# Kernel optimization log

Hardware: AMD Instinct MI355X
Metric: run time of the kernel (lower is better)

Reference implementation:

```python
import jax, jax.numpy as jnp
import numpy as np

NUM_ROUTES = 32
LN_EPS = 1e-5


def _ln(x, g, b):
    mu = jnp.mean(x, axis=-1, keepdims=True)
    var = jnp.mean(jnp.square(x - mu), axis=-1, keepdims=True)
    return (x - mu) * jax.lax.rsqrt(var + LN_EPS) * g + b


def setup_inputs() -> dict:
    key = jax.random.key(0)
    ks = jax.random.split(key, 16)
    B, N, D = 64, 512, 512
    s = 1.0 / np.sqrt(D)
    return {
        "tokens": jax.random.normal(ks[0], (B, N, D), jnp.float32),
        "token_mask": jax.random.bernoulli(ks[1], 0.7, (B, N)),
        "route_ids": jax.random.randint(ks[2], (N,), 0, NUM_ROUTES),
        # token_ffn: LayerNorm + Linear(D,4D) + GELU + Linear(4D,D)
        "ln1_g": jnp.ones((D,), jnp.float32),
        "ln1_b": jnp.zeros((D,), jnp.float32),
        "w1": jax.random.normal(ks[3], (D, 4 * D), jnp.float32) * s,
        "b1": jnp.zeros((4 * D,), jnp.float32),
        "w2": jax.random.normal(ks[4], (4 * D, D), jnp.float32) * (0.5 * s),
        "b2": jnp.zeros((D,), jnp.float32),
        # within_route_pool: LayerNorm + Linear(D,1)
        "wp_g": jnp.ones((D,), jnp.float32),
        "wp_b": jnp.zeros((D,), jnp.float32),
        "wp_w": jax.random.normal(ks[5], (D,), jnp.float32) * s,
        "wp_bias": jnp.zeros((), jnp.float32),
        # route_pool: LayerNorm + Linear(D,1)
        "rp_g": jnp.ones((D,), jnp.float32),
        "rp_b": jnp.zeros((D,), jnp.float32),
        "rp_w": jax.random.normal(ks[6], (D,), jnp.float32) * s,
        "rp_bias": jnp.zeros((), jnp.float32),
    }


def reference(tokens, token_mask, route_ids, ln1_g, ln1_b, w1, b1, w2, b2,
              wp_g, wp_b, wp_w, wp_bias, rp_g, rp_b, rp_w, rp_bias):
    # token FFN with residual (dropout=0 in eval path)
    h = _ln(tokens, ln1_g, ln1_b)
    h = jax.nn.gelu(h @ w1 + b1, approximate=False)
    x = tokens + (h @ w2 + b2)                       # [B, N, D]

    # within-route attention pool: score is mask-independent -> compute once
    tok_logits = _ln(x, wp_g, wp_b) @ wp_w + wp_bias  # [B, N]

    route_onehot = route_ids[None, :] == jnp.arange(NUM_ROUTES)[:, None]  # [R, N]
    mask = route_onehot[None, :, :] & token_mask[:, None, :]              # [B, R, N]

    ml = jnp.where(mask, tok_logits[:, None, :], -1e9)
    w = jax.nn.softmax(ml, axis=-1)
    w = jnp.where(mask, w, 0.0)
    w = w / jnp.maximum(jnp.sum(w, axis=-1, keepdims=True), 1e-6)
    routes = jnp.einsum('brn,bnd->brd', w, x)         # [B, R, D]
    present = jnp.any(mask, axis=-1)                  # [B, R]

    # route-level attention pool
    rl = _ln(routes, rp_g, rp_b) @ rp_w + rp_bias     # [B, R]
    rl = jnp.where(present, rl, -1e9)
    rw = jax.nn.softmax(rl, axis=-1)
    rw = jnp.where(present, rw, 0.0)
    rw = rw / jnp.maximum(jnp.sum(rw, axis=-1, keepdims=True), 1e-6)
    return jnp.einsum('br,brd->bd', rw, routes)       # [B, D]
```

## Files before the change

kernel.cpp:

```cpp
#include <hip/hip_runtime.h>
#include <hip/hip_bf16.h>
#include <math.h>

#define B_ 64
#define N_ 512
#define D_ 512
#define H_ 2048
#define R_ 32
#define M_ (B_ * N_)

typedef __bf16 bf16x8 __attribute__((ext_vector_type(8)));
typedef float f32x4 __attribute__((ext_vector_type(4)));

__device__ __forceinline__ void async_ld16(const void* g, void* l) {
  __builtin_amdgcn_global_load_lds((__attribute__((address_space(1))) void*)g,
                                   (__attribute__((address_space(3))) void*)l,
                                   16, 0, 0);
}

__device__ __forceinline__ float fast_gelu(float v) {
  const float s = v * 0.70710678118654752f;
  const float a = fabsf(s);
  const float t = 1.0f / fmaf(0.3275911f, a, 1.0f);
  const float poly = t * fmaf(t, fmaf(t, fmaf(t, fmaf(t, 1.061405429f, -1.453152027f),
                                              1.421413741f), -0.284496736f), 0.254829592f);
  const float er = 1.0f - poly * __expf(-a * a);
  const float erfs = (s >= 0.f) ? er : -er;
  return 0.5f * v * (1.0f + erfs);
}

__global__ void mask_detect_kernel(const unsigned char* __restrict__ raw,
                                   int* __restrict__ flag) {
  __shared__ int f;
  if (threadIdx.x == 0) f = 0;
  __syncthreads();
  const uint4* p = (const uint4*)raw;
  unsigned acc = 0;
  for (int k = threadIdx.x; k < M_ / 16; k += 256) {
    const uint4 v = p[k];
    acc |= (v.x | v.y | v.z | v.w) & 0xFFFFFF00u;
  }
  if (acc) f = 1;
  __syncthreads();
  if (threadIdx.x == 0) flag[0] = f;
}

__global__ __launch_bounds__(256) void transpose_cast_kernel(
    const float* __restrict__ src, __hip_bfloat16* __restrict__ dst, int R, int C) {
  __shared__ float tile[64][65];
  const int c0 = blockIdx.x * 64, r0 = blockIdx.y * 64;
  const int tx = threadIdx.x & 63, ty = threadIdx.x >> 6;
  for (int r = ty; r < 64; r += 4)
    tile[r][tx] = src[(size_t)(r0 + r) * C + c0 + tx];
  __syncthreads();
  for (int r = ty; r < 64; r += 4)
    dst[(size_t)(c0 + r) * R + r0 + tx] = __float2bfloat16(tile[tx][r]);
}

__global__ __launch_bounds__(512) void ln_rows_kernel(
    const float* __restrict__ src, const float* __restrict__ gw,
    const float* __restrict__ gb, __hip_bfloat16* __restrict__ dst) {
  const int wv = threadIdx.x >> 6, lane = threadIdx.x & 63;
  const int row = blockIdx.x * 8 + wv;
  const float* p = src + (size_t)row * D_ + lane * 8;
  const float4 v0 = *(const float4*)p;
  const float4 v1 = *(const float4*)(p + 4);
  float s = v0.x + v0.y + v0.z + v0.w + v1.x + v1.y + v1.z + v1.w;
  float ss = v0.x * v0.x + v0.y * v0.y + v0.z * v0.z + v0.w * v0.w +
             v1.x * v1.x + v1.y * v1.y + v1.z * v1.z + v1.w * v1.w;
#pragma unroll
  for (int m = 32; m > 0; m >>= 1) {
    s += __shfl_xor(s, m);
    ss += __shfl_xor(ss, m);
  }
  const float mu = s * (1.0f / D_);
  const float rstd = rsqrtf(ss * (1.0f / D_) - mu * mu + 1e-5f);
  const float4 g0 = *(const float4*)(gw + lane * 8);
  const float4 g1 = *(const float4*)(gw + lane * 8 + 4);
  const float4 b0 = *(const float4*)(gb + lane * 8);
  const float4 b1 = *(const float4*)(gb + lane * 8 + 4);
  const float vv[8] = {v0.x, v0.y, v0.z, v0.w, v1.x, v1.y, v1.z, v1.w};
  const float gg[8] = {g0.x, g0.y, g0.z, g0.w, g1.x, g1.y, g1.z, g1.w};
  const float bb[8] = {b0.x, b0.y, b0.z, b0.w, b1.x, b1.y, b1.z, b1.w};
  union { __hip_bfloat16 h[8]; uint4 u; } pk;
#pragma unroll
  for (int t = 0; t < 8; ++t)
    pk.h[t] = __float2bfloat16((vv[t] - mu) * rstd * gg[t] + bb[t]);
  *(uint4*)(dst + (size_t)row * D_ + lane * 8) = pk.u;
}

__global__ __launch_bounds__(256, 2) void gemm_bias_gelu_kernel(
    const __hip_bfloat16* __restrict__ A, const __hip_bfloat16* __restrict__ Bt,
    const float* __restrict__ bias, __hip_bfloat16* __restrict__ C,
    int K, int ldc, int NC) {
  __shared__ alignas(16) unsigned short SU[8192];
  unsigned short* As = SU;
  unsigned short* Bs = SU + 4096;
  const int tid = threadIdx.x;
  const int w = tid >> 6;
  const int lane = tid & 63;
  const int bid = blockIdx.x;
  const int rowT = (bid / (NC * 8)) * 8 + (bid & 7);
  const int colT = (bid >> 3) % NC;
  const int rowBase = rowT * 128;
  const int colBase = colT * 128;
  const int warpRow = w >> 1;
  const int warpCol = w & 1;
  const int q = lane >> 4;
  const int mr = lane & 15;
  const int srow = lane >> 2;
  const int skc = (((lane & 3) ^ ((srow >> 1) & 3))) * 8;
  const int jsA = q ^ ((mr >> 1) & 3);

  f32x4 acc[4][4] = {};

  for (int k0 = 0; k0 < K; k0 += 32) {
    __syncthreads();
#pragma unroll
    for (int i = 0; i < 2; ++i) {
      const int c = i * 4 + w;
      const int row = c * 16 + srow;
      async_ld16(&A[(size_t)(rowBase + row) * K + (k0 + skc)], (void*)&As[c * 512]);
      async_ld16(&Bt[(size_t)(colBase + row) * K + (k0 + skc)], (void*)&Bs[c * 512]);
    }
    __syncthreads();
    bf16x8 af[4], bf[4];
#pragma unroll
    for (int i = 0; i < 4; ++i)
      af[i] = *reinterpret_cast<const bf16x8*>(&As[(warpRow * 64 + i * 16 + mr) * 32 + jsA * 8]);
#pragma unroll
    for (int j = 0; j < 4; ++j)
      bf[j] = *reinterpret_cast<const bf16x8*>(&Bs[(warpCol * 64 + j * 16 + mr) * 32 + jsA * 8]);
#pragma unroll
    for (int i = 0; i < 4; ++i)
#pragma unroll
      for (int j = 0; j < 4; ++j)
        acc[i][j] = __builtin_amdgcn_mfma_f32_16x16x32_bf16(af[i], bf[j], acc[i][j], 0, 0, 0);
  }

  __hip_bfloat16* SB = (__hip_bfloat16*)SU;
  const int lg = tid & 15;
  const int rsub = tid >> 4;
#pragma unroll
  for (int p = 0; p < 2; ++p) {
    __syncthreads();
    if (warpRow == p) {
#pragma unroll
      for (int j = 0; j < 4; ++j) {
        const int n = warpCol * 64 + j * 16 + mr;
        const float bv = bias[colBase + n];
        const int g16 = n >> 4;
#pragma unroll
        for (int i = 0; i < 4; ++i) {
#pragma unroll
          for (int r = 0; r < 4; ++r) {
            const int m = i * 16 + q * 4 + r;
            SB[m * 128 + ((g16 ^ (m & 7)) << 4) + (n & 15)] =
                __float2bfloat16(fast_gelu(acc[i][j][r] + bv));
          }
        }
      }
    }
    __syncthreads();
#pragma unroll
    for (int it = 0; it < 4; ++it) {
      const int m = it * 16 + rsub;
      const int pg = (lg >> 1) ^ (m & 7);
      const uint4 val = *(const uint4*)&SB[m * 128 + (pg << 4) + (lg & 1) * 8];
      *(uint4*)&C[(size_t)(rowBase + p * 64 + m) * ldc + colBase + lg * 8] = val;
    }
  }
}

__global__ __launch_bounds__(256, 2) void gemm_acc_kernel(
    const __hip_bfloat16* __restrict__ A, const __hip_bfloat16* __restrict__ Bt,
    const float* __restrict__ bias, const float* __restrict__ resid,
    float* __restrict__ X, int K, int ldb, int first) {
  __shared__ alignas(16) unsigned short SU[8192];
  unsigned short* As = SU;
  unsigned short* Bs = SU + 4096;
  const int tid = threadIdx.x;
  const int w = tid >> 6;
  const int lane = tid & 63;
  const int bid = blockIdx.x;
  const int NC = 4;
  const int rowT = (bid / (NC * 8)) * 8 + (bid & 7);
  const int colT = (bid >> 3) % NC;
  const int rowBase = rowT * 128;
  const int colBase = colT * 128;
  const int warpRow = w >> 1;
  const int warpCol = w & 1;
  const int q = lane >> 4;
  const int mr = lane & 15;
  const int srow = lane >> 2;
  const int skc = (((lane & 3) ^ ((srow >> 1) & 3))) * 8;
  const int jsA = q ^ ((mr >> 1) & 3);

  f32x4 acc[4][4] = {};

  for (int k0 = 0; k0 < K; k0 += 32) {
    __syncthreads();
#pragma unroll
    for (int i = 0; i < 2; ++i) {
      const int c = i * 4 + w;
      const int row = c * 16 + srow;
      async_ld16(&A[(size_t)(rowBase + row) * K + (k0 + skc)], (void*)&As[c * 512]);
      async_ld16(&Bt[(size_t)(colBase + row) * ldb + (k0 + skc)], (void*)&Bs[c * 512]);
    }
    __syncthreads();
    bf16x8 af[4], bf[4];
#pragma unroll
    for (int i = 0; i < 4; ++i)
      af[i] = *reinterpret_cast<const bf16x8*>(&As[(warpRow * 64 + i * 16 + mr) * 32 + jsA * 8]);
#pragma unroll
    for (int j = 0; j < 4; ++j)
      bf[j] = *reinterpret_cast<const bf16x8*>(&Bs[(warpCol * 64 + j * 16 + mr) * 32 + jsA * 8]);
#pragma unroll
    for (int i = 0; i < 4; ++i)
#pragma unroll
      for (int j = 0; j < 4; ++j)
        acc[i][j] = __builtin_amdgcn_mfma_f32_16x16x32_bf16(af[i], bf[j], acc[i][j], 0, 0, 0);
  }

#pragma unroll
  for (int j = 0; j < 4; ++j) {
    const int n = colBase + warpCol * 64 + j * 16 + mr;
    const float bv = bias[n];
#pragma unroll
    for (int i = 0; i < 4; ++i) {
#pragma unroll
      for (int r = 0; r < 4; ++r) {
        const int m = rowBase + warpRow * 64 + i * 16 + q * 4 + r;
        const size_t idx = (size_t)m * N_ + n;
        const float base = first ? (resid[idx] + bv) : X[idx];
        X[idx] = base + acc[i][j][r];
      }
    }
  }
}

__global__ __launch_bounds__(256) void route_pool_kernel(
    const float* __restrict__ X, const int* __restrict__ route_ids,
    const void* __restrict__ mask_raw, const int* __restrict__ flag,
    const float* __restrict__ gw, const float* __restrict__ gb,
    const float* __restrict__ ww, const float* __restrict__ wbias,
    float* __restrict__ routes, int* __restrict__ present) {
  const int b = blockIdx.x >> 5;
  const int r = blockIdx.x & 31;
  const int tid = threadIdx.x;
  __shared__ int cnt;
  __shared__ int ls[N_];
  __shared__ float lw[N_];
  if (tid == 0) cnt = 0;
  __syncthreads();
  const int fl = flag[0];
  for (int n = tid; n < N_; n += 256) {
    const int mk = fl ? (int)((const unsigned char*)mask_raw)[b * N_ + n]
                      : ((const int*)mask_raw)[b * N_ + n];
    if (route_ids[n] == r && mk != 0) {
      int p = atomicAdd(&cnt, 1);
      ls[p] = n;
    }
  }
  __syncthreads();
  const int c = cnt;
  const int wv = tid >> 6, lane = tid & 63;
  for (int t = wv; t < c; t += 4) {
    const float* p = X + ((size_t)b * N_ + ls[t]) * D_ + lane * 8;
    const float4 v0 = *(const float4*)p;
    const float4 v1 = *(const float4*)(p + 4);
    float s = v0.x + v0.y + v0.z + v0.w + v1.x + v1.y + v1.z + v1.w;
    float ss = v0.x * v0.x + v0.y * v0.y + v0.z * v0.z + v0.w * v0.w +
               v1.x * v1.x + v1.y * v1.y + v1.z * v1.z + v1.w * v1.w;
#pragma unroll
    for (int m = 32; m > 0; m >>= 1) {
      s += __shfl_xor(s, m);
      ss += __shfl_xor(ss, m);
    }
    const float mu = s * (1.0f / D_);
    const float rstd = rsqrtf(ss * (1.0f / D_) - mu * mu + 1e-5f);
    const float4 g0 = *(const float4*)(gw + lane * 8);
    const float4 g1 = *(const float4*)(gw + lane * 8 + 4);
    const float4 b0 = *(const float4*)(gb + lane * 8);
    const float4 b1 = *(const float4*)(gb + lane * 8 + 4);
    const float4 w0 = *(const float4*)(ww + lane * 8);
    const float4 w1 = *(const float4*)(ww + lane * 8 + 4);
    const float vv[8] = {v0.x, v0.y, v0.z, v0.w, v1.x, v1.y, v1.z, v1.w};
    const float gg[8] = {g0.x, g0.y, g0.z, g0.w, g1.x, g1.y, g1.z, g1.w};
    const float bb[8] = {b0.x, b0.y, b0.z, b0.w, b1.x, b1.y, b1.z, b1.w};
    const float wwv[8] = {w0.x, w0.y, w0.z, w0.w, w1.x, w1.y, w1.z, w1.w};
    float a = 0.f;
#pragma unroll
    for (int t2 = 0; t2 < 8; ++t2) a += ((vv[t2] - mu) * rstd * gg[t2] + bb[t2]) * wwv[t2];
#pragma unroll
    for (int m = 32; m > 0; m >>= 1) a += __shfl_xor(a, m);
    if (lane == 0) lw[t] = a + wbias[0];
  }
  __syncthreads();
  if (tid == 0 && c > 0) {
    float mx = -1e30f;
    for (int i = 0; i < c; ++i) mx = fmaxf(mx, lw[i]);
    float sm = 0.f;
    for (int i = 0; i < c; ++i) {
      const float e = __expf(lw[i] - mx);
      lw[i] = e;
      sm += e;
    }
    const float inv = 1.0f / sm;
    for (int i = 0; i < c; ++i) lw[i] *= inv;
  }
  __syncthreads();
  float a0 = 0.f, a1 = 0.f;
  for (int i = 0; i < c; ++i) {
    const float* xr = X + ((size_t)b * N_ + ls[i]) * D_;
    const float wgt = lw[i];
    a0 += wgt * xr[tid];
    a1 += wgt * xr[tid + 256];
  }
  float* outp = routes + ((size_t)b * R_ + r) * D_;
  outp[tid] = a0;
  outp[tid + 256] = a1;
  if (tid == 0) present[b * R_ + r] = (c > 0) ? 1 : 0;
}

__global__ __launch_bounds__(512) void final_pool_kernel(
    const float* __restrict__ routes, const int* __restrict__ present,
    const float* __restrict__ gw, const float* __restrict__ gb,
    const float* __restrict__ ww, const float* __restrict__ wbias,
    float* __restrict__ out) {
  const int b = blockIdx.x;
  const int wv = threadIdx.x >> 6, lane = threadIdx.x & 63;
  __shared__ float srw[R_];
  __shared__ float srl[R_];
  for (int r = wv; r < R_; r += 8) {
    const float* p = routes + ((size_t)b * R_ + r) * D_ + lane * 8;
    const float4 v0 = *(const float4*)p;
    const float4 v1 = *(const float4*)(p + 4);
    float s = v0.x + v0.y + v0.z + v0.w + v1.x + v1.y + v1.z + v1.w;
    float ss = v0.x * v0.x + v0.y * v0.y + v0.z * v0.z + v0.w * v0.w +
               v1.x * v1.x + v1.y * v1.y + v1.z * v1.z + v1.w * v1.w;
#pragma unroll
    for (int m = 32; m > 0; m >>= 1) {
      s += __shfl_xor(s, m);
      ss += __shfl_xor(ss, m);
    }
    const float mu = s * (1.0f / D_);
    const float rstd = rsqrtf(ss * (1.0f / D_) - mu * mu + 1e-5f);
    const float4 g0 = *(const float4*)(gw + lane * 8);
    const float4 g1 = *(const float4*)(gw + lane * 8 + 4);
    const float4 b0 = *(const float4*)(gb + lane * 8);
    const float4 b1 = *(const float4*)(gb + lane * 8 + 4);
    const float4 w0 = *(const float4*)(ww + lane * 8);
    const float4 w1 = *(const float4*)(ww + lane * 8 + 4);
    const float vv[8] = {v0.x, v0.y, v0.z, v0.w, v1.x, v1.y, v1.z, v1.w};
    const float gg[8] = {g0.x, g0.y, g0.z, g0.w, g1.x, g1.y, g1.z, g1.w};
    const float bb[8] = {b0.x, b0.y, b0.z, b0.w, b1.x, b1.y, b1.z, b1.w};
    const float wwv[8] = {w0.x, w0.y, w0.z, w0.w, w1.x, w1.y, w1.z, w1.w};
    float a = 0.f;
#pragma unroll
    for (int t = 0; t < 8; ++t) a += ((vv[t] - mu) * rstd * gg[t] + bb[t]) * wwv[t];
#pragma unroll
    for (int m = 32; m > 0; m >>= 1) a += __shfl_xor(a, m);
    if (lane == 0) srl[r] = a + wbias[0];
  }
  __syncthreads();
  if (threadIdx.x == 0) {
    float mx = -1e30f;
    for (int r = 0; r < R_; ++r)
      if (present[b * R_ + r]) mx = fmaxf(mx, srl[r]);
    float sm = 0.f;
    for (int r = 0; r < R_; ++r) {
      const float e = present[b * R_ + r] ? __expf(srl[r] - mx) : 0.f;
      srw[r] = e;
      sm += e;
    }
    const float inv = (sm > 0.f) ? 1.0f / sm : 0.f;
    for (int r = 0; r < R_; ++r) srw[r] *= inv;
  }
  __syncthreads();
  const int d = threadIdx.x;
  float a = 0.f;
  for (int r = 0; r < R_; ++r) a += srw[r] * routes[((size_t)b * R_ + r) * D_ + d];
  out[(size_t)b * D_ + d] = a;
}

extern "C" void kernel_launch(void* const* d_in, const int* in_sizes, int n_in,
                              void* d_out, int out_size, void* d_ws, size_t ws_size,
                              hipStream_t stream) {
  const float* tokens = (const float*)d_in[0];
  const void* mask_raw = d_in[1];
  const int* route_ids = (const int*)d_in[2];
  const float* ln1_g = (const float*)d_in[3];
  const float* ln1_b = (const float*)d_in[4];
  const float* w1 = (const float*)d_in[5];
  const float* b1 = (const float*)d_in[6];
  const float* w2 = (const float*)d_in[7];
  const float* b2 = (const float*)d_in[8];
  const float* wp_g = (const float*)d_in[9];
  const float* wp_b = (const float*)d_in[10];
  const float* wp_w = (const float*)d_in[11];
  const float* wp_bias = (const float*)d_in[12];
  const float* rp_g = (const float*)d_in[13];
  const float* rp_b = (const float*)d_in[14];
  const float* rp_w = (const float*)d_in[15];
  const float* rp_bias = (const float*)d_in[16];
  float* out = (float*)d_out;

  char* ws = (char*)d_ws;
  size_t off = 0;
  auto carve = [&](size_t bytes) -> void* {
    void* p = ws + off;
    off = (off + bytes + 255) & ~(size_t)255;
    return p;
  };

  __hip_bfloat16* w1t = (__hip_bfloat16*)carve((size_t)H_ * D_ * 2);
  __hip_bfloat16* w2t = (__hip_bfloat16*)carve((size_t)D_ * H_ * 2);
  __hip_bfloat16* aBf = (__hip_bfloat16*)carve((size_t)M_ * D_ * 2);
  float* X = (float*)carve((size_t)M_ * D_ * 4);
  int* flag = (int*)carve(256);
  int* present = (int*)carve((size_t)B_ * R_ * 4);
  float* routes = (float*)carve((size_t)B_ * R_ * D_ * 4);

  int G = 1;
  while (G < 16 && off + (size_t)M_ * (H_ / G) * 2 > ws_size) G <<= 1;
  const int Hg = H_ / G;
  __hip_bfloat16* hbuf = (__hip_bfloat16*)carve((size_t)M_ * Hg * 2);

  mask_detect_kernel<<<1, 256, 0, stream>>>((const unsigned char*)mask_raw, flag);
  transpose_cast_kernel<<<dim3(H_ / 64, D_ / 64), 256, 0, stream>>>(w1, w1t, D_, H_);
  transpose_cast_kernel<<<dim3(D_ / 64, H_ / 64), 256, 0, stream>>>(w2, w2t, H_, D_);
  ln_rows_kernel<<<M_ / 8, 512, 0, stream>>>(tokens, ln1_g, ln1_b, aBf);

  const int NC1 = Hg / 128;
  for (int g = 0; g < G; ++g) {
    gemm_bias_gelu_kernel<<<(M_ / 128) * NC1, 256, 0, stream>>>(
        aBf, w1t + (size_t)g * Hg * D_, b1 + (size_t)g * Hg, hbuf, D_, Hg, NC1);
    gemm_acc_kernel<<<(M_ / 128) * 4, 256, 0, stream>>>(
        hbuf, w2t + (size_t)g * Hg, b2, tokens, X, Hg, H_, (g == 0) ? 1 : 0);
  }

  route_pool_kernel<<<B_ * R_, 256, 0, stream>>>(
      X, route_ids, mask_raw, flag, wp_g, wp_b, wp_w, wp_bias, routes, present);
  final_pool_kernel<<<B_, 512, 0, stream>>>(routes, present, rp_g, rp_b, rp_w, rp_bias, out);
}
```

Before: 429.2 us.

## Fuse FFN up-projection, GELU and down-projection into one on-chip kernel

Adds a fused FFN kernel in which each block keeps a 128-row bf16 LayerNorm tile in LDS. It computes the hidden layer in 64-column chunks, applies bias and GELU into a swizzled LDS buffer, and accumulates the down-projection in registers before writing the residual output. This removes the large bf16 hidden-activation buffer and its global write and read round trip, plus the repeated kernel launches. The price is a single-wave grid of 256 blocks, heavy register accumulators, weight operands loaded directly from global or L2 without LDS staging, and about 146 KB of LDS per block, which limits occupancy to one block per CU. The old two-GEMM path is kept as a fallback when the LDS size check fails.

```diff
diff --git a/kernel.cpp b/kernel.cpp
--- a/kernel.cpp
+++ b/kernel.cpp
@@ -87,6 +87,103 @@
   for (int t = 0; t < 8; ++t)
     pk.h[t] = __float2bfloat16((vv[t] - mu) * rstd * gg[t] + bb[t]);
   *(uint4*)(dst + (size_t)row * D_ + lane * 8) = pk.u;
+}
+
+#define ASTRIDE 520
+#define FUSED_LDS ((128 * ASTRIDE + 128 * 64) * 2)
+
+__global__ __launch_bounds__(512, 2) void ffn_fused_kernel(
+    const __hip_bfloat16* __restrict__ aBf,
+    const __hip_bfloat16* __restrict__ w1t,
+    const __hip_bfloat16* __restrict__ w2t,
+    const float* __restrict__ b1,
+    const float* __restrict__ b2,
+    const float* __restrict__ resid,
+    float* __restrict__ X) {
+  extern __shared__ unsigned short smem[];
+  unsigned short* Als = smem;
+  unsigned short* Hls = smem + 128 * ASTRIDE;
+  const int tid = threadIdx.x;
+  const int w = tid >> 6;
+  const int lane = tid & 63;
+  const int q = lane >> 4, mr = lane & 15;
+  const int rowBase = blockIdx.x * 128;
+  const int hr = w >> 2;
+  const int hc = w & 3;
+
+  {
+    const __hip_bfloat16* src = aBf + (size_t)rowBase * 512;
+#pragma unroll
+    for (int rr = 0; rr < 16; ++rr) {
+      const int row = w * 16 + rr;
+      async_ld16(src + (size_t)row * 512 + lane * 8, (void*)&Als[row * ASTRIDE]);
+    }
+  }
+  f32x4 accX[4][8] = {};
+  __syncthreads();
+
+  for (int ch = 0; ch < 32; ++ch) {
+    const int cb = ch * 64;
+    f32x4 accH[4] = {};
+    const __hip_bfloat16* w1p = w1t + (size_t)(cb + hc * 16 + mr) * 512 + q * 8;
+#pragma unroll
+    for (int s = 0; s < 16; ++s) {
+      const bf16x8 bw = *(const bf16x8*)(w1p + s * 32);
+#pragma unroll
+      for (int i = 0; i < 4; ++i) {
+        const bf16x8 af =
+            *(const bf16x8*)&Als[(hr * 64 + i * 16 + mr) * ASTRIDE + s * 32 + q * 8];
+        accH[i] = __builtin_amdgcn_mfma_f32_16x16x32_bf16(af, bw, accH[i], 0, 0, 0);
+      }
+    }
+    const float bv = b1[cb + hc * 16 + mr];
+    __syncthreads();
+#pragma unroll
+    for (int i = 0; i < 4; ++i) {
+#pragma unroll
+      for (int r = 0; r < 4; ++r) {
+        const int row = hr * 64 + i * 16 + q * 4 + r;
+        const int col = hc * 16 + mr;
+        const int slot = (col >> 3) ^ (row & 7);
+        const __hip_bfloat16 hv = __float2bfloat16(fast_gelu(accH[i][r] + bv));
+        Hls[row * 64 + slot * 8 + (col & 7)] = *(const unsigned short*)&hv;
+      }
+    }
+    __syncthreads();
+    const __hip_bfloat16* w2p = w2t + (size_t)(hc * 128 + mr) * 2048 + cb + q * 8;
+#pragma unroll
+    for (int s = 0; s < 2; ++s) {
+      bf16x8 aH[4];
+#pragma unroll
+      for (int i = 0; i < 4; ++i) {
+        const int row = hr * 64 + i * 16 + mr;
+        const int slot = (s * 4 + q) ^ (mr & 7);
+        aH[i] = *(const bf16x8*)&Hls[row * 64 + slot * 8];
+      }
+#pragma unroll
+      for (int j = 0; j < 8; ++j) {
+        const bf16x8 bw2 = *(const bf16x8*)(w2p + (size_t)(j * 16) * 2048 + s * 32);
+#pragma unroll
+        for (int i = 0; i < 4; ++i)
+          accX[i][j] = __builtin_amdgcn_mfma_f32_16x16x32_bf16(aH[i], bw2, accX[i][j], 0, 0, 0);
+      }
+    }
+  }
+
+#pragma unroll
+  for (int j = 0; j < 8; ++j) {
+    const int n = hc * 128 + j * 16 + mr;
+    const float bvo = b2[n];
+#pragma unroll
+    for (int i = 0; i < 4; ++i) {
+#pragma unroll
+      for (int r = 0; r < 4; ++r) {
+        const int m = rowBase + hr * 64 + i * 16 + q * 4 + r;
+        const size_t idx = (size_t)m * 512 + n;
+        X[idx] = resid[idx] + bvo + accX[i][j][r];
+      }
+    }
+  }
 }
 
 __global__ __launch_bounds__(256, 2) void gemm_bias_gelu_kernel(
@@ -282,13 +379,13 @@
     const float4 g0 = *(const float4*)(gw + lane * 8);
     const float4 g1 = *(const float4*)(gw + lane * 8 + 4);
     const float4 b0 = *(const float4*)(gb + lane * 8);
-    const float4 b1 = *(const float4*)(gb + lane * 8 + 4);
+    const float4 b1v = *(const float4*)(gb + lane * 8 + 4);
     const float4 w0 = *(const float4*)(ww + lane * 8);
-    const float4 w1 = *(const float4*)(ww + lane * 8 + 4);
+    const float4 w1v = *(const float4*)(ww + lane * 8 + 4);
     const float vv[8] = {v0.x, v0.y, v0.z, v0.w, v1.x, v1.y, v1.z, v1.w};
     const float gg[8] = {g0.x, g0.y, g0.z, g0.w, g1.x, g1.y, g1.z, g1.w};
-    const float bb[8] = {b0.x, b0.y, b0.z, b0.w, b1.x, b1.y, b1.z, b1.w};
-    const float wwv[8] = {w0.x, w0.y, w0.z, w0.w, w1.x, w1.y, w1.z, w1.w};
+    const float bb[8] = {b0.x, b0.y, b0.z, b0.w, b1v.x, b1v.y, b1v.z, b1v.w};
+    const float wwv[8] = {w0.x, w0.y, w0.z, w0.w, w1v.x, w1v.y, w1v.z, w1v.w};
     float a = 0.f;
 #pragma unroll
     for (int t2 = 0; t2 < 8; ++t2) a += ((vv[t2] - mu) * rstd * gg[t2] + bb[t2]) * wwv[t2];
@@ -349,13 +446,13 @@
     const float4 g0 = *(const float4*)(gw + lane * 8);
     const float4 g1 = *(const float4*)(gw + lane * 8 + 4);
     const float4 b0 = *(const float4*)(gb + lane * 8);
-    const float4 b1 = *(const float4*)(gb + lane * 8 + 4);
+    const float4 b1v = *(const float4*)(gb + lane * 8 + 4);
     const float4 w0 = *(const float4*)(ww + lane * 8);
-    const float4 w1 = *(const float4*)(ww + lane * 8 + 4);
+    const float4 w1v = *(const float4*)(ww + lane * 8 + 4);
     const float vv[8] = {v0.x, v0.y, v0.z, v0.w, v1.x, v1.y, v1.z, v1.w};
     const float gg[8] = {g0.x, g0.y, g0.z, g0.w, g1.x, g1.y, g1.z, g1.w};
-    const float bb[8] = {b0.x, b0.y, b0.z, b0.w, b1.x, b1.y, b1.z, b1.w};
-    const float wwv[8] = {w0.x, w0.y, w0.z, w0.w, w1.x, w1.y, w1.z, w1.w};
+    const float bb[8] = {b0.x, b0.y, b0.z, b0.w, b1v.x, b1v.y, b1v.z, b1v.w};
+    const float wwv[8] = {w0.x, w0.y, w0.z, w0.w, w1v.x, w1v.y, w1v.z, w1v.w};
     float a = 0.f;
 #pragma unroll
     for (int t = 0; t < 8; ++t) a += ((vv[t] - mu) * rstd * gg[t] + bb[t]) * wwv[t];
@@ -422,22 +519,44 @@
   int* present = (int*)carve((size_t)B_ * R_ * 4);
   float* routes = (float*)carve((size_t)B_ * R_ * D_ * 4);
 
-  int G = 1;
-  while (G < 16 && off + (size_t)M_ * (H_ / G) * 2 > ws_size) G <<= 1;
-  const int Hg = H_ / G;
-  __hip_bfloat16* hbuf = (__hip_bfloat16*)carve((size_t)M_ * Hg * 2);
+  bool fused_ok = false;
+  {
+    int maxShmPerMP = 0;
+    if (hipDeviceGetAttribute(&maxShmPerMP,
+                              hipDeviceAttributeMaxSharedMemoryPerMultiprocessor,
+                              0) == hipSuccess &&
+        maxShmPerMP >= FUSED_LDS) {
+      (void)hipFuncSetAttribute((const void*)ffn_fused_kernel,
+                                hipFuncAttributeMaxDynamicSharedMemorySize,
+                                FUSED_LDS);
+      int nb = 0;
+      if (hipOccupancyMaxActiveBlocksPerMultiprocessor(
+              &nb, ffn_fused_kernel, 512, (size_t)FUSED_LDS) == hipSuccess &&
+          nb >= 1)
+        fused_ok = true;
+    }
+  }
 
   mask_detect_kernel<<<1, 256, 0, stream>>>((const unsigned char*)mask_raw, flag);
   transpose_cast_kernel<<<dim3(H_ / 64, D_ / 64), 256, 0, stream>>>(w1, w1t, D_, H_);
   transpose_cast_kernel<<<dim3(D_ / 64, H_ / 64), 256, 0, stream>>>(w2, w2t, H_, D_);
   ln_rows_kernel<<<M_ / 8, 512, 0, stream>>>(tokens, ln1_g, ln1_b, aBf);
 
-  const int NC1 = Hg / 128;
-  for (int g = 0; g < G; ++g) {
-    gemm_bias_gelu_kernel<<<(M_ / 128) * NC1, 256, 0, stream>>>(
-        aBf, w1t + (size_t)g * Hg * D_, b1 + (size_t)g * Hg, hbuf, D_, Hg, NC1);
-    gemm_acc_kernel<<<(M_ / 128) * 4, 256, 0, stream>>>(
-        hbuf, w2t + (size_t)g * Hg, b2, tokens, X, Hg, H_, (g == 0) ? 1 : 0);
+  if (fused_ok) {
+    ffn_fused_kernel<<<M_ / 128, 512, FUSED_LDS, stream>>>(
+        aBf, w1t, w2t, b1, b2, tokens, X);
+  } else {
+    int G = 1;
+    while (G < 16 && off + (size_t)M_ * (H_ / G) * 2 > ws_size) G <<= 1;
+    const int Hg = H_ / G;
+    __hip_bfloat16* hbuf = (__hip_bfloat16*)carve((size_t)M_ * Hg * 2);
+    const int NC1 = Hg / 128;
+    for (int g = 0; g < G; ++g) {
+      gemm_bias_gelu_kernel<<<(M_ / 128) * NC1, 256, 0, stream>>>(
+          aBf, w1t + (size_t)g * Hg * D_, b1 + (size_t)g * Hg, hbuf, D_, Hg, NC1);
+      gemm_acc_kernel<<<(M_ / 128) * 4, 256, 0, stream>>>(
+          hbuf, w2t + (size_t)g * Hg, b2, tokens, X, Hg, H_, (g == 0) ? 1 : 0);
+    }
   }
 
   route_pool_kernel<<<B_ * R_, 256, 0, stream>>>(
```

Result: no change. 422.1 us (-1.7%).

## Merge prep kernels into one launch and simplify GEMM1 epilogue to single pass

Applied to the files above, without the earlier changes.

Combines the mask-detect, two weight transpose-casts and the LayerNorm-to-bf16 pass into one block-dispatched prep kernel, which removes three kernel launches. The first GEMM's epilogue now stages the whole 128x128 output tile in doubled shared memory and writes it back in one pass instead of two synchronized halves, using a new XOR swizzle. GELU uses a hardware reciprocal in place of a division. The larger shared-memory footprint may reduce occupancy for the GEMM kernel.

```diff
diff --git a/kernel.cpp b/kernel.cpp
--- a/kernel.cpp
+++ b/kernel.cpp
@@ -21,79 +21,85 @@
 __device__ __forceinline__ float fast_gelu(float v) {
   const float s = v * 0.70710678118654752f;
   const float a = fabsf(s);
-  const float t = 1.0f / fmaf(0.3275911f, a, 1.0f);
+  const float t = __builtin_amdgcn_rcpf(fmaf(0.3275911f, a, 1.0f));
   const float poly = t * fmaf(t, fmaf(t, fmaf(t, fmaf(t, 1.061405429f, -1.453152027f),
                                               1.421413741f), -0.284496736f), 0.254829592f);
   const float er = 1.0f - poly * __expf(-a * a);
-  const float erfs = (s >= 0.f) ? er : -er;
-  return 0.5f * v * (1.0f + erfs);
-}
-
-__global__ void mask_detect_kernel(const unsigned char* __restrict__ raw,
-                                   int* __restrict__ flag) {
-  __shared__ int f;
-  if (threadIdx.x == 0) f = 0;
-  __syncthreads();
-  const uint4* p = (const uint4*)raw;
-  unsigned acc = 0;
-  for (int k = threadIdx.x; k < M_ / 16; k += 256) {
-    const uint4 v = p[k];
-    acc |= (v.x | v.y | v.z | v.w) & 0xFFFFFF00u;
-  }
-  if (acc) f = 1;
-  __syncthreads();
-  if (threadIdx.x == 0) flag[0] = f;
-}
-
-__global__ __launch_bounds__(256) void transpose_cast_kernel(
-    const float* __restrict__ src, __hip_bfloat16* __restrict__ dst, int R, int C) {
-  __shared__ float tile[64][65];
-  const int c0 = blockIdx.x * 64, r0 = blockIdx.y * 64;
-  const int tx = threadIdx.x & 63, ty = threadIdx.x >> 6;
-  for (int r = ty; r < 64; r += 4)
-    tile[r][tx] = src[(size_t)(r0 + r) * C + c0 + tx];
-  __syncthreads();
-  for (int r = ty; r < 64; r += 4)
-    dst[(size_t)(c0 + r) * R + r0 + tx] = __float2bfloat16(tile[tx][r]);
-}
-
-__global__ __launch_bounds__(512) void ln_rows_kernel(
-    const float* __restrict__ src, const float* __restrict__ gw,
-    const float* __restrict__ gb, __hip_bfloat16* __restrict__ dst) {
-  const int wv = threadIdx.x >> 6, lane = threadIdx.x & 63;
-  const int row = blockIdx.x * 8 + wv;
-  const float* p = src + (size_t)row * D_ + lane * 8;
-  const float4 v0 = *(const float4*)p;
-  const float4 v1 = *(const float4*)(p + 4);
-  float s = v0.x + v0.y + v0.z + v0.w + v1.x + v1.y + v1.z + v1.w;
-  float ss = v0.x * v0.x + v0.y * v0.y + v0.z * v0.z + v0.w * v0.w +
-             v1.x * v1.x + v1.y * v1.y + v1.z * v1.z + v1.w * v1.w;
-#pragma unroll
-  for (int m = 32; m > 0; m >>= 1) {
-    s += __shfl_xor(s, m);
-    ss += __shfl_xor(ss, m);
-  }
-  const float mu = s * (1.0f / D_);
-  const float rstd = rsqrtf(ss * (1.0f / D_) - mu * mu + 1e-5f);
-  const float4 g0 = *(const float4*)(gw + lane * 8);
-  const float4 g1 = *(const float4*)(gw + lane * 8 + 4);
-  const float4 b0 = *(const float4*)(gb + lane * 8);
-  const float4 b1 = *(const float4*)(gb + lane * 8 + 4);
-  const float vv[8] = {v0.x, v0.y, v0.z, v0.w, v1.x, v1.y, v1.z, v1.w};
-  const float gg[8] = {g0.x, g0.y, g0.z, g0.w, g1.x, g1.y, g1.z, g1.w};
-  const float bb[8] = {b0.x, b0.y, b0.z, b0.w, b1.x, b1.y, b1.z, b1.w};
-  union { __hip_bfloat16 h[8]; uint4 u; } pk;
-#pragma unroll
-  for (int t = 0; t < 8; ++t)
-    pk.h[t] = __float2bfloat16((vv[t] - mu) * rstd * gg[t] + bb[t]);
-  *(uint4*)(dst + (size_t)row * D_ + lane * 8) = pk.u;
+  return 0.5f * v * (1.0f + ((s >= 0.f) ? er : -er));
+}
+
+__global__ __launch_bounds__(512) void prep_kernel(
+    const float* __restrict__ tokens, const void* __restrict__ mask_raw,
+    const float* __restrict__ ln1_g, const float* __restrict__ ln1_b,
+    const float* __restrict__ w1, const float* __restrict__ w2,
+    __hip_bfloat16* __restrict__ aBf, __hip_bfloat16* __restrict__ w1t,
+    __hip_bfloat16* __restrict__ w2t, int* __restrict__ flag) {
+  const int bid = blockIdx.x;
+  const int tid = threadIdx.x;
+  if (bid == 0) {
+    __shared__ int f;
+    if (tid == 0) f = 0;
+    __syncthreads();
+    const uint4* p = (const uint4*)mask_raw;
+    unsigned acc = 0;
+    for (int k = tid; k < M_ / 16; k += 512) {
+      const uint4 v = p[k];
+      acc |= (v.x | v.y | v.z | v.w) & 0xFFFFFF00u;
+    }
+    if (acc) f = 1;
+    __syncthreads();
+    if (tid == 0) flag[0] = f;
+  } else if (bid <= 512) {
+    __shared__ float tile[64][65];
+    const int t = bid - 1;
+    const float* src;
+    __hip_bfloat16* dst;
+    int R, C, cx, ry;
+    if (t < 256) { src = w1; dst = w1t; R = 512; C = 2048; cx = t & 31; ry = t >> 5; }
+    else { const int t2 = t - 256; src = w2; dst = w2t; R = 2048; C = 512; cx = t2 & 7; ry = t2 >> 3; }
+    const int c0 = cx * 64, r0 = ry * 64;
+    const int tx = tid & 63, ty = tid >> 6;
+    for (int r = ty; r < 64; r += 8)
+      tile[r][tx] = src[(size_t)(r0 + r) * C + c0 + tx];
+    __syncthreads();
+    for (int r = ty; r < 64; r += 8)
+      dst[(size_t)(c0 + r) * R + r0 + tx] = __float2bfloat16(tile[tx][r]);
+  } else {
+    const int wv = tid >> 6, lane = tid & 63;
+    const int row = (bid - 513) * 8 + wv;
+    const float* p = tokens + (size_t)row * D_ + lane * 8;
+    const float4 v0 = *(const float4*)p;
+    const float4 v1 = *(const float4*)(p + 4);
+    float s = v0.x + v0.y + v0.z + v0.w + v1.x + v1.y + v1.z + v1.w;
+    float ss = v0.x * v0.x + v0.y * v0.y + v0.z * v0.z + v0.w * v0.w +
+               v1.x * v1.x + v1.y * v1.y + v1.z * v1.z + v1.w * v1.w;
+#pragma unroll
+    for (int m = 32; m > 0; m >>= 1) {
+      s += __shfl_xor(s, m);
+      ss += __shfl_xor(ss, m);
+    }
+    const float mu = s * (1.0f / D_);
+    const float rstd = rsqrtf(ss * (1.0f / D_) - mu * mu + 1e-5f);
+    const float4 g0 = *(const float4*)(ln1_g + lane * 8);
+    const float4 g1 = *(const float4*)(ln1_g + lane * 8 + 4);
+    const float4 b0 = *(const float4*)(ln1_b + lane * 8);
+    const float4 b1 = *(const float4*)(ln1_b + lane * 8 + 4);
+    const float vv[8] = {v0.x, v0.y, v0.z, v0.w, v1.x, v1.y, v1.z, v1.w};
+    const float gg[8] = {g0.x, g0.y, g0.z, g0.w, g1.x, g1.y, g1.z, g1.w};
+    const float bb[8] = {b0.x, b0.y, b0.z, b0.w, b1.x, b1.y, b1.z, b1.w};
+    union { __hip_bfloat16 h[8]; uint4 u; } pk;
+#pragma unroll
+    for (int t2 = 0; t2 < 8; ++t2)
+      pk.h[t2] = __float2bfloat16((vv[t2] - mu) * rstd * gg[t2] + bb[t2]);
+    *(uint4*)(aBf + (size_t)row * D_ + lane * 8) = pk.u;
+  }
 }
 
 __global__ __launch_bounds__(256, 2) void gemm_bias_gelu_kernel(
     const __hip_bfloat16* __restrict__ A, const __hip_bfloat16* __restrict__ Bt,
     const float* __restrict__ bias, __hip_bfloat16* __restrict__ C,
     int K, int ldc, int NC) {
-  __shared__ alignas(16) unsigned short SU[8192];
+  __shared__ alignas(16) unsigned short SU[16384];
   unsigned short* As = SU;
   unsigned short* Bs = SU + 4096;
   const int tid = threadIdx.x;
@@ -138,37 +144,31 @@
         acc[i][j] = __builtin_amdgcn_mfma_f32_16x16x32_bf16(af[i], bf[j], acc[i][j], 0, 0, 0);
   }
 
+  __syncthreads();
   __hip_bfloat16* SB = (__hip_bfloat16*)SU;
-  const int lg = tid & 15;
-  const int rsub = tid >> 4;
-#pragma unroll
-  for (int p = 0; p < 2; ++p) {
-    __syncthreads();
-    if (warpRow == p) {
-#pragma unroll
-      for (int j = 0; j < 4; ++j) {
-        const int n = warpCol * 64 + j * 16 + mr;
-        const float bv = bias[colBase + n];
-        const int g16 = n >> 4;
-#pragma unroll
-        for (int i = 0; i < 4; ++i) {
-#pragma unroll
-          for (int r = 0; r < 4; ++r) {
-            const int m = i * 16 + q * 4 + r;
-            SB[m * 128 + ((g16 ^ (m & 7)) << 4) + (n & 15)] =
-                __float2bfloat16(fast_gelu(acc[i][j][r] + bv));
-          }
-        }
+#pragma unroll
+  for (int j = 0; j < 4; ++j) {
+    const int col = warpCol * 64 + j * 16 + mr;
+    const float bv = bias[colBase + col];
+#pragma unroll
+    for (int i = 0; i < 4; ++i) {
+#pragma unroll
+      for (int r = 0; r < 4; ++r) {
+        const int row = warpRow * 64 + i * 16 + q * 4 + r;
+        const int slot = (col >> 3) ^ (row & 7);
+        SB[row * 128 + slot * 8 + (col & 7)] =
+            __float2bfloat16(fast_gelu(acc[i][j][r] + bv));
       }
     }
-    __syncthreads();
-#pragma unroll
-    for (int it = 0; it < 4; ++it) {
-      const int m = it * 16 + rsub;
-      const int pg = (lg >> 1) ^ (m & 7);
-      const uint4 val = *(const uint4*)&SB[m * 128 + (pg << 4) + (lg & 1) * 8];
-      *(uint4*)&C[(size_t)(rowBase + p * 64 + m) * ldc + colBase + lg * 8] = val;
-    }
+  }
+  __syncthreads();
+  const int lg = tid & 15, rsub = tid >> 4;
+#pragma unroll
+  for (int it = 0; it < 8; ++it) {
+    const int m = it * 16 + rsub;
+    const int slot = lg ^ (m & 7);
+    const uint4 val = *(const uint4*)&SB[m * 128 + slot * 8];
+    *(uint4*)&C[(size_t)(rowBase + m) * ldc + colBase + lg * 8] = val;
   }
 }
 
@@ -282,13 +282,13 @@
     const float4 g0 = *(const float4*)(gw + lane * 8);
     const float4 g1 = *(const float4*)(gw + lane * 8 + 4);
     const float4 b0 = *(const float4*)(gb + lane * 8);
-    const float4 b1 = *(const float4*)(gb + lane * 8 + 4);
+    const float4 b1v = *(const float4*)(gb + lane * 8 + 4);
     const float4 w0 = *(const float4*)(ww + lane * 8);
-    const float4 w1 = *(const float4*)(ww + lane * 8 + 4);
+    const float4 w1v = *(const float4*)(ww + lane * 8 + 4);
     const float vv[8] = {v0.x, v0.y, v0.z, v0.w, v1.x, v1.y, v1.z, v1.w};
     const float gg[8] = {g0.x, g0.y, g0.z, g0.w, g1.x, g1.y, g1.z, g1.w};
-    const float bb[8] = {b0.x, b0.y, b0.z, b0.w, b1.x, b1.y, b1.z, b1.w};
-    const float wwv[8] = {w0.x, w0.y, w0.z, w0.w, w1.x, w1.y, w1.z, w1.w};
+    const float bb[8] = {b0.x, b0.y, b0.z, b0.w, b1v.x, b1v.y, b1v.z, b1v.w};
+    const float wwv[8] = {w0.x, w0.y, w0.z, w0.w, w1v.x, w1v.y, w1v.z, w1v.w};
     float a = 0.f;
 #pragma unroll
     for (int t2 = 0; t2 < 8; ++t2) a += ((vv[t2] - mu) * rstd * gg[t2] + bb[t2]) * wwv[t2];
@@ -349,13 +349,13 @@
     const float4 g0 = *(const float4*)(gw + lane * 8);
     const float4 g1 = *(const float4*)(gw + lane * 8 + 4);
     const float4 b0 = *(const float4*)(gb + lane * 8);
-    const float4 b1 = *(const float4*)(gb + lane * 8 + 4);
+    const float4 b1v = *(const float4*)(gb + lane * 8 + 4);
     const float4 w0 = *(const float4*)(ww + lane * 8);
-    const float4 w1 = *(const float4*)(ww + lane * 8 + 4);
+    const float4 w1v = *(const float4*)(ww + lane * 8 + 4);
     const float vv[8] = {v0.x, v0.y, v0.z, v0.w, v1.x, v1.y, v1.z, v1.w};
     const float gg[8] = {g0.x, g0.y, g0.z, g0.w, g1.x, g1.y, g1.z, g1.w};
-    const float bb[8] = {b0.x, b0.y, b0.z, b0.w, b1.x, b1.y, b1.z, b1.w};
-    const float wwv[8] = {w0.x, w0.y, w0.z, w0.w, w1.x, w1.y, w1.z, w1.w};
+    const float bb[8] = {b0.x, b0.y, b0.z, b0.w, b1v.x, b1v.y, b1v.z, b1v.w};
+    const float wwv[8] = {w0.x, w0.y, w0.z, w0.w, w1v.x, w1v.y, w1v.z, w1v.w};
     float a = 0.f;
 #pragma unroll
     for (int t = 0; t < 8; ++t) a += ((vv[t] - mu) * rstd * gg[t] + bb[t]) * wwv[t];
@@ -427,10 +427,8 @@
   const int Hg = H_ / G;
   __hip_bfloat16* hbuf = (__hip_bfloat16*)carve((size_t)M_ * Hg * 2);
 
-  mask_detect_kernel<<<1, 256, 0, stream>>>((const unsigned char*)mask_raw, flag);
-  transpose_cast_kernel<<<dim3(H_ / 64, D_ / 64), 256, 0, stream>>>(w1, w1t, D_, H_);
-  transpose_cast_kernel<<<dim3(D_ / 64, H_ / 64), 256, 0, stream>>>(w2, w2t, H_, D_);
-  ln_rows_kernel<<<M_ / 8, 512, 0, stream>>>(tokens, ln1_g, ln1_b, aBf);
+  prep_kernel<<<513 + M_ / 8, 512, 0, stream>>>(
+      tokens, mask_raw, ln1_g, ln1_b, w1, w2, aBf, w1t, w2t, flag);
 
   const int NC1 = Hg / 128;
   for (int g = 0; g < G; ++g) {
```

New measurement: 368.2 us. 14.2% less time.
